# Performance work log

Measured on AMD Instinct MI355X. Metric: run time of the kernel, lower is better.

Reference implementation:

```python
import jax, jax.numpy as jnp
import numpy as np

N = 100000      # nodes
E = 1600000     # edges (before self-loops)
F_IN = 128      # dataset.num_features
H1 = 128        # hidden_channels/2
H2 = 256        # hidden_channels
C = 40          # dataset.num_classes
EPS = 1e-5      # BatchNorm eps
NEG_SLOPE = 0.2 # GATConv leaky_relu slope


def setup_inputs() -> dict:
    key = jax.random.key(0)
    ks = jax.random.split(key, 12)
    p = lambda k, shape: jax.random.normal(k, shape, jnp.float32) * 0.1
    x = jax.random.normal(ks[0], (N, F_IN), jnp.float32)
    edge_index = jax.random.randint(ks[1], (2, E), 0, N, dtype=jnp.int64)
    return dict(
        x=x, edge_index=edge_index,
        w1=p(ks[2], (F_IN, H1)), as1=p(ks[3], (H1,)), ad1=p(ks[4], (H1,)), b1=jnp.zeros(H1, jnp.float32),
        g1=jnp.ones(H1, jnp.float32), be1=jnp.zeros(H1, jnp.float32), rm1=jnp.zeros(H1, jnp.float32), rv1=jnp.ones(H1, jnp.float32),
        w2=p(ks[5], (H1, H2)), as2=p(ks[6], (H2,)), ad2=p(ks[7], (H2,)), b2=jnp.zeros(H2, jnp.float32),
        g2=jnp.ones(H2, jnp.float32), be2=jnp.zeros(H2, jnp.float32), rm2=jnp.zeros(H2, jnp.float32), rv2=jnp.ones(H2, jnp.float32),
        w3=p(ks[8], (H2, C)), as3=p(ks[9], (C,)), ad3=p(ks[10], (C,)), b3=jnp.zeros(C, jnp.float32),
    )


def gat_conv(x, src, dst, W, a_src, a_dst, b):
    """PyG GATConv (heads=1, add_self_loops already applied to src/dst)."""
    h = x @ W                                  # [N, F_out]
    alpha_src = h @ a_src                      # [N]
    alpha_dst = h @ a_dst                      # [N]
    logits = jax.nn.leaky_relu(alpha_src[src] + alpha_dst[dst], NEG_SLOPE)  # [E']
    # segment softmax over incoming edges of each dst node
    m = jax.ops.segment_max(logits, dst, num_segments=N)
    e = jnp.exp(logits - m[dst])
    denom = jax.ops.segment_sum(e, dst, num_segments=N)
    alpha = e / denom[dst]                     # [E']
    out = jax.ops.segment_sum(h[src] * alpha[:, None], dst, num_segments=N)
    return out + b


def bn_eval(x, gamma, beta, mean, var):
    return (x - mean) * jax.lax.rsqrt(var + EPS) * gamma + beta


def reference(x, edge_index,
              w1, as1, ad1, b1, g1, be1, rm1, rv1,
              w2, as2, ad2, b2, g2, be2, rm2, rv2,
              w3, as3, ad3, b3):
    # add self-loops once (PyG GATConv default add_self_loops=True)
    loop = jnp.arange(N, dtype=edge_index.dtype)
    src = jnp.concatenate([edge_index[0], loop])
    dst = jnp.concatenate([edge_index[1], loop])
    # eval mode: dropout is identity, BN uses running stats
    h = gat_conv(x, src, dst, w1, as1, ad1, b1)
    h = jnp.tanh(bn_eval(h, g1, be1, rm1, rv1))
    h = gat_conv(h, src, dst, w2, as2, ad2, b2)
    h = jnp.tanh(bn_eval(h, g2, be2, rm2, rv2))
    return gat_conv(h, src, dst, w3, as3, ad3, b3)
```

## Files before the change

### kernel.cpp

```cpp
#include <hip/hip_runtime.h>
#include <hip/hip_bf16.h>
#include <cstddef>

#define N_NODES 100000
#define E_EDGES 1600000
#define TOT_EDGES (E_EDGES + N_NODES)
#define NEG_SLOPE 0.2f
#define BN_EPS 1e-5f
#define NBKT ((N_NODES + 255) / 256)
#define NBA 512

typedef __attribute__((ext_vector_type(8))) short short8;
typedef __attribute__((ext_vector_type(4))) float f32x4;
typedef __attribute__((ext_vector_type(2))) float f32x2;
typedef __attribute__((ext_vector_type(4))) int int32x4;
typedef __attribute__((ext_vector_type(2))) int int32x2;

#if defined(__has_builtin)
#if __has_builtin(__builtin_amdgcn_make_buffer_rsrc) && __has_builtin(__builtin_amdgcn_raw_buffer_load_b128)
#define HAVE_BUFRSRC 1
#endif
#if __has_builtin(__builtin_amdgcn_make_buffer_rsrc) && __has_builtin(__builtin_amdgcn_raw_buffer_load_b64)
#define HAVE_BUF64 1
#endif
#endif

__device__ __forceinline__ unsigned short f2bf(float f) {
    union { float f; unsigned u; } c; c.f = f;
    unsigned u = c.u;
    u += 0x7fffu + ((u >> 16) & 1u);
    return (unsigned short)(u >> 16);
}
__device__ __forceinline__ float bf2f(unsigned short h) {
    union { unsigned u; float f; } c; c.u = ((unsigned)h) << 16;
    return c.f;
}
__device__ __forceinline__ unsigned short f2h(float f) {
    union { _Float16 h; unsigned short u; } c; c.h = (_Float16)f; return c.u;
}
__device__ __forceinline__ float lrelu(float t) {
    return (t > 0.f) ? t : NEG_SLOPE * t;
}
__device__ __forceinline__ float tanh_fast(float x) {
    float e = __expf(2.f * x);
    return 1.f - 2.f / (e + 1.f);
}
__device__ __forceinline__ unsigned short pk_fp8(float a, float b) {
    unsigned v;
    asm volatile("v_cvt_pk_fp8_f32 %0, %1, %2" : "=v"(v) : "v"(a), "v"(b));
    return (unsigned short)v;
}
__device__ __forceinline__ f32x2 unpk_fp8(unsigned u) {
    f32x2 r;
    asm volatile("v_cvt_pk_f32_fp8 %0, %1" : "=v"(r) : "v"(u));
    return r;
}

__device__ __forceinline__ float wave_sum63(float x) {
    x += __int_as_float(__builtin_amdgcn_update_dpp(0, __float_as_int(x), 0x111, 0xf, 0xf, true));
    x += __int_as_float(__builtin_amdgcn_update_dpp(0, __float_as_int(x), 0x112, 0xf, 0xf, true));
    x += __int_as_float(__builtin_amdgcn_update_dpp(0, __float_as_int(x), 0x114, 0xf, 0xf, true));
    x += __int_as_float(__builtin_amdgcn_update_dpp(0, __float_as_int(x), 0x118, 0xf, 0xf, true));
    x += __int_as_float(__builtin_amdgcn_update_dpp(0, __float_as_int(x), 0x142, 0xf, 0xf, true));
    x += __int_as_float(__builtin_amdgcn_update_dpp(0, __float_as_int(x), 0x143, 0xf, 0xf, true));
    return x;
}
__device__ __forceinline__ float wave_sum_bcast(float x) {
    return __int_as_float(__builtin_amdgcn_readlane(__float_as_int(wave_sum63(x)), 63));
}


__global__ __launch_bounds__(256) void csr_hist(const int* __restrict__ ei,
                                                int* __restrict__ bh) {
    __shared__ int h[NBKT];
    int t = threadIdx.x;
    for (int b = t; b < NBKT; b += 256) h[b] = 0;
    __syncthreads();
    int idx = blockIdx.x * 256 + t;
    const int stride = NBA * 256;
    for (int e = idx; e < TOT_EDGES; e += stride) {
        int d = (e < E_EDGES) ? ei[E_EDGES + e] : (e - E_EDGES);
        atomicAdd(&h[((unsigned)d) >> 8], 1);
    }
    __syncthreads();
    for (int b = t; b < NBKT; b += 256) bh[blockIdx.x * NBKT + b] = h[b];
}

__global__ __launch_bounds__(512) void csr_scan_blocks(int* __restrict__ bh,
                                                       int* __restrict__ totals) {
    __shared__ int s[NBA];
    int t = threadIdx.x, bin = blockIdx.x;
    int v = bh[t * NBKT + bin];
    s[t] = v;
    __syncthreads();
    for (int off = 1; off < NBA; off <<= 1) {
        int y = (t >= off) ? s[t - off] : 0;
        __syncthreads();
        s[t] += y;
        __syncthreads();
    }
    bh[t * NBKT + bin] = s[t] - v;
    if (t == NBA - 1) totals[bin] = s[t];
}

__global__ __launch_bounds__(512) void csr_scan_buckets(const int* __restrict__ totals,
                                                        int* __restrict__ starts) {
    __shared__ int s[512];
    int t = threadIdx.x;
    int v = (t < NBKT) ? totals[t] : 0;
    s[t] = v;
    __syncthreads();
    for (int off = 1; off < 512; off <<= 1) {
        int y = (t >= off) ? s[t - off] : 0;
        __syncthreads();
        s[t] += y;
        __syncthreads();
    }
    if (t < NBKT) starts[t] = s[t] - v;
    if (t == 0) starts[NBKT] = TOT_EDGES;
}

__global__ __launch_bounds__(256) void csr_scatter(const int* __restrict__ ei,
                                                   const int* __restrict__ bh,
                                                   const int* __restrict__ starts,
                                                   int* __restrict__ pairs) {
    __shared__ int wp[NBKT];
    int t = threadIdx.x;
    for (int b = t; b < NBKT; b += 256)
        wp[b] = starts[b] + bh[blockIdx.x * NBKT + b];
    __syncthreads();
    int idx = blockIdx.x * 256 + t;
    const int stride = NBA * 256;
    for (int e = idx; e < TOT_EDGES; e += stride) {
        int s, d;
        if (e < E_EDGES) { s = ei[e]; d = ei[E_EDGES + e]; }
        else             { s = e - E_EDGES; d = s; }
        int pos = atomicAdd(&wp[((unsigned)d) >> 8], 1);
        pairs[pos] = s | ((d & 255) << 20);
    }
}

__global__ __launch_bounds__(256) void csr_build(const int* __restrict__ pairs,
                                                 const int* __restrict__ starts,
                                                 int* __restrict__ row_ptr,
                                                 int* __restrict__ src_sorted) {
    __shared__ int nh[256];
    __shared__ int sc[256];
    __shared__ int wp[256];
    int k = blockIdx.x, t = threadIdx.x;
    int bs = starts[k], be = starts[k + 1];
    nh[t] = 0;
    __syncthreads();
    for (int i = bs + t; i < be; i += 256)
        atomicAdd(&nh[((unsigned)pairs[i]) >> 20], 1);
    __syncthreads();
    int v = nh[t];
    sc[t] = v;
    __syncthreads();
    for (int off = 1; off < 256; off <<= 1) {
        int y = (t >= off) ? sc[t - off] : 0;
        __syncthreads();
        sc[t] += y;
        __syncthreads();
    }
    int excl = sc[t] - v;
    int node = k * 256 + t;
    if (node <= N_NODES) row_ptr[node] = bs + excl;
    wp[t] = bs + excl;
    __syncthreads();
    for (int i = bs + t; i < be; i += 256) {
        unsigned p = (unsigned)pairs[i];
        int pos = atomicAdd(&wp[p >> 20], 1);
        src_sorted[pos] = (int)(p & 0xFFFFFu);
    }
}

__global__ __launch_bounds__(256) void wprep_all(
    const float* __restrict__ w1, const float* __restrict__ w2, const float* __restrict__ w3,
    const float* __restrict__ as1, const float* __restrict__ ad1,
    const float* __restrict__ as2, const float* __restrict__ ad2,
    const float* __restrict__ as3, const float* __restrict__ ad3,
    unsigned short* __restrict__ w1th, unsigned short* __restrict__ w1tl,
    unsigned short* __restrict__ w2th, unsigned short* __restrict__ w2tl,
    unsigned short* __restrict__ w3th, unsigned short* __restrict__ w3tl,
    unsigned short* __restrict__ ab1h, unsigned short* __restrict__ ab1l,
    unsigned short* __restrict__ ab3h, unsigned short* __restrict__ ab3l,
    float* __restrict__ ws2f, float* __restrict__ wd2f) {
    const int T1 = 128 * 128, T2 = 256 * 128, T3 = 48 * 256;
    const int W = T1 + T2 + T3;
    int idx = blockIdx.x * 256 + threadIdx.x;
    if (idx < W) {
        float v; unsigned short* th; unsigned short* tl; int o;
        if (idx < T1) {
            int n = idx / 128, k = idx % 128;
            v = w1[k * 128 + n]; th = w1th; tl = w1tl; o = idx;
        } else if (idx < T1 + T2) {
            int i = idx - T1; int n = i / 128, k = i % 128;
            v = w2[k * 256 + n]; th = w2th; tl = w2tl; o = i;
        } else {
            int i = idx - T1 - T2; int n = i / 256, k = i % 256;
            v = (n < 40) ? w3[k * 40 + n] : 0.f; th = w3th; tl = w3tl; o = i;
        }
        unsigned short h = f2bf(v);
        th[o] = h;
        tl[o] = f2bf(v - bf2f(h));
        return;
    }
    int j = idx - W;
    if (j < 2048) {
        int r = j / 128, k = j % 128;
        float v = 0.f;
        if (r < 2) {
            const float* a = r ? ad1 : as1;
            const float* wr = w1 + (size_t)k * 128;
            for (int n = 0; n < 128; n++) v += wr[n] * a[n];
        }
        unsigned short h = f2bf(v);
        ab1h[j] = h; ab1l[j] = f2bf(v - bf2f(h));
    } else if (j < 2048 + 4096) {
        int i = j - 2048; int r = i / 256, k = i % 256;
        float v = 0.f;
        if (r < 2) {
            const float* a = r ? ad3 : as3;
            const float* wr = w3 + (size_t)k * 40;
            for (int n = 0; n < 40; n++) v += wr[n] * a[n];
        }
        unsigned short h = f2bf(v);
        ab3h[i] = h; ab3l[i] = f2bf(v - bf2f(h));
    } else if (j < 2048 + 4096 + 256) {
        int i = j - 2048 - 4096; int r = i / 128, k = i % 128;
        const float* a = r ? ad2 : as2;
        const float* wr = w2 + (size_t)k * 256;
        float v = 0.f;
        for (int n = 0; n < 256; n++) v += wr[n] * a[n];
        if (r == 0) ws2f[k] = v; else wd2f[k] = v;
    }
}

template<int K, int NTILES, int MWAVES, int NWAVES, int NACT, bool ASPLIT, bool ALPHA, bool BNT, bool CFRAG, bool CHALF, bool AF32>
__global__ __launch_bounds__(256) void mfma_gemm(
    const unsigned short* __restrict__ Ahi, const unsigned short* __restrict__ Alo,
    const unsigned short* __restrict__ BThi, const unsigned short* __restrict__ BTlo,
    const unsigned short* __restrict__ ABh, const unsigned short* __restrict__ ABl,
    unsigned short* __restrict__ Chi, int ldc,
    const float* __restrict__ bias, const float* __restrict__ gamma,
    const float* __restrict__ beta, const float* __restrict__ rmean,
    const float* __restrict__ rvar,
    float* __restrict__ asrc, float* __restrict__ adst, int M)
{
    int lane = threadIdx.x & 63;
    int wave = threadIdx.x >> 6;
    int quad = lane >> 4;
    int l16  = lane & 15;
    long mbase = (long)blockIdx.x * (64 * MWAVES) + (long)(wave / NWAVES) * 64;
    int n0 = ((wave % NWAVES) + blockIdx.y * NWAVES) * (NTILES * 16);
    bool aw = ((wave % NWAVES) == 0) && (blockIdx.y == 0);
    const size_t CSTRIDE = (size_t)M * 32;

    size_t roff[4];
#pragma unroll
    for (int i = 0; i < 4; i++) {
        long r = mbase + i * 16 + l16;
        if (r > M - 1) r = M - 1;
        roff[i] = AF32 ? ((size_t)r * K + (size_t)(quad * 8))
                       : ((size_t)r * 32 + (size_t)(quad * 8));
    }
    const unsigned short* bh[NTILES]; const unsigned short* bl[NTILES];
#pragma unroll
    for (int j = 0; j < NTILES; j++) {
        long n = n0 + j * 16 + l16;
        bh[j] = BThi + n * K; bl[j] = BTlo + n * K;
    }
    const unsigned short* bah = nullptr; const unsigned short* bal = nullptr;
    if constexpr (ALPHA) { bah = ABh + (size_t)l16 * K; bal = ABl + (size_t)l16 * K; }
    const int ko = quad * 8;

    f32x4 acc[4][NTILES];
    f32x4 acca[4];
#pragma unroll
    for (int i = 0; i < 4; i++) {
        acca[i] = (f32x4){0.f, 0.f, 0.f, 0.f};
#pragma unroll
        for (int j = 0; j < NTILES; j++)
            acc[i][j] = (f32x4){0.f, 0.f, 0.f, 0.f};
    }

    for (int kc = 0; kc < K / 32; kc++) {
        const int k0 = kc * 32;
        short8 vah[4], vall[4], vbh[NTILES], vbl[NTILES];
#pragma unroll
        for (int i = 0; i < 4; i++) {
            if constexpr (AF32) {
                const float* xf = (const float*)Ahi;
                const float* pa = xf + roff[i] + kc * 32;
                f32x4 va = *(const f32x4*)pa;
                f32x4 vb = *(const f32x4*)(pa + 4);
#pragma unroll
                for (int q = 0; q < 8; q++) {
                    float v = (q < 4) ? va[q] : vb[q - 4];
                    unsigned short h = f2bf(v);
                    vah[i][q] = (short)h;
                    vall[i][q] = (short)f2bf(v - bf2f(h));
                }
            } else {
                const unsigned short* Ah = Ahi + (size_t)kc * CSTRIDE;
                vah[i] = *(const short8*)(Ah + roff[i]);
                if constexpr (ASPLIT) {
                    const unsigned short* Al = Alo + (size_t)kc * CSTRIDE;
                    vall[i] = *(const short8*)(Al + roff[i]);
                }
            }
        }
#pragma unroll
        for (int j = 0; j < NTILES; j++) {
            vbh[j] = *(const short8*)(bh[j] + k0 + ko);
            vbl[j] = *(const short8*)(bl[j] + k0 + ko);
        }
#pragma unroll
        for (int i = 0; i < 4; i++)
#pragma unroll
            for (int j = 0; j < NTILES; j++) {
                acc[i][j] = __builtin_amdgcn_mfma_f32_16x16x32_bf16(vah[i], vbh[j], acc[i][j], 0, 0, 0);
                acc[i][j] = __builtin_amdgcn_mfma_f32_16x16x32_bf16(vah[i], vbl[j], acc[i][j], 0, 0, 0);
                if constexpr (ASPLIT)
                    acc[i][j] = __builtin_amdgcn_mfma_f32_16x16x32_bf16(vall[i], vbh[j], acc[i][j], 0, 0, 0);
            }
        if constexpr (ALPHA) {
            if (aw) {
                short8 vbah = *(const short8*)(bah + k0 + ko);
                short8 vbal = *(const short8*)(bal + k0 + ko);
#pragma unroll
                for (int i = 0; i < 4; i++) {
                    acca[i] = __builtin_amdgcn_mfma_f32_16x16x32_bf16(vah[i], vbah, acca[i], 0, 0, 0);
                    acca[i] = __builtin_amdgcn_mfma_f32_16x16x32_bf16(vah[i], vbal, acca[i], 0, 0, 0);
                    if constexpr (ASPLIT)
                        acca[i] = __builtin_amdgcn_mfma_f32_16x16x32_bf16(vall[i], vbah, acca[i], 0, 0, 0);
                }
            }
        }
    }

#pragma unroll
    for (int i = 0; i < 4; i++)
#pragma unroll
        for (int j = 0; j < NTILES; j++) {
            int col = n0 + j * 16 + l16;
            float bb = 0.f, rs = 1.f, gg = 1.f, bt = 0.f, rm = 0.f;
            if constexpr (BNT) {
                bb = bias[col]; gg = gamma[col]; bt = beta[col];
                rm = rmean[col]; rs = rsqrtf(rvar[col] + BN_EPS);
            }
#pragma unroll
            for (int r = 0; r < 4; r++) {
                long row = mbase + i * 16 + quad * 4 + r;
                if (row < M && col < NACT) {
                    float v = acc[i][j][r];
                    if constexpr (BNT) v = tanh_fast((v + bb - rm) * rs * gg + bt);
                    if constexpr (CFRAG) {
                        Chi[(size_t)(col >> 5) * CSTRIDE + (size_t)row * 32 + (col & 31)] = f2bf(v);
                    } else {
                        Chi[row * ldc + col] = CHALF ? f2h(v) : f2bf(v);
                    }
                }
            }
        }
    if constexpr (ALPHA) {
        if (aw) {
#pragma unroll
            for (int i = 0; i < 4; i++)
#pragma unroll
                for (int r = 0; r < 4; r++) {
                    long row = mbase + i * 16 + quad * 4 + r;
                    if (row < M) {
                        float v = acca[i][r];
                        if (l16 == 0) asrc[row] = v;
                        else if (l16 == 1) adst[row] = v;
                    }
                }
        }
    }
}

__global__ __launch_bounds__(256) void gemm23_fused(
    const unsigned short* __restrict__ Ahi,
    const unsigned short* __restrict__ B2h, const unsigned short* __restrict__ B2l,
    const float* __restrict__ bias, const float* __restrict__ gamma,
    const float* __restrict__ beta, const float* __restrict__ rmean,
    const float* __restrict__ rvar,
    const unsigned short* __restrict__ B3h, const unsigned short* __restrict__ B3l,
    const unsigned short* __restrict__ AB3h, const unsigned short* __restrict__ AB3l,
    unsigned short* __restrict__ h3,
    float* __restrict__ asrc, float* __restrict__ adst, int M)
{
    constexpr int LW = 40;
    __shared__ unsigned short o2l[8 * 64 * LW];

    int lane = threadIdx.x & 63;
    int wave = threadIdx.x >> 6;
    int quad = lane >> 4;
    int l16  = lane & 15;
    long mbase = (long)blockIdx.x * 64;
    const size_t CSTRIDE = (size_t)M * 32;
    const int ko = quad * 8;

    size_t roff[4];
#pragma unroll
    for (int i = 0; i < 4; i++) {
        long r = mbase + i * 16 + l16;
        if (r > M - 1) r = M - 1;
        roff[i] = (size_t)r * 32 + (size_t)ko;
    }
    int n0 = wave * 64;
    const unsigned short* bh[4]; const unsigned short* bl[4];
#pragma unroll
    for (int j = 0; j < 4; j++) {
        long n = n0 + j * 16 + l16;
        bh[j] = B2h + n * 128; bl[j] = B2l + n * 128;
    }

    f32x4 acc[4][4];
#pragma unroll
    for (int i = 0; i < 4; i++)
#pragma unroll
        for (int j = 0; j < 4; j++)
            acc[i][j] = (f32x4){0.f, 0.f, 0.f, 0.f};

    for (int kc = 0; kc < 4; kc++) {
        const int k0 = kc * 32;
        const unsigned short* Ah = Ahi + (size_t)kc * CSTRIDE;
        short8 vah[4], vbh[4], vbl[4];
#pragma unroll
        for (int i = 0; i < 4; i++) vah[i] = *(const short8*)(Ah + roff[i]);
#pragma unroll
        for (int j = 0; j < 4; j++) {
            vbh[j] = *(const short8*)(bh[j] + k0 + ko);
            vbl[j] = *(const short8*)(bl[j] + k0 + ko);
        }
#pragma unroll
        for (int i = 0; i < 4; i++)
#pragma unroll
            for (int j = 0; j < 4; j++) {
                acc[i][j] = __builtin_amdgcn_mfma_f32_16x16x32_bf16(vah[i], vbh[j], acc[i][j], 0, 0, 0);
                acc[i][j] = __builtin_amdgcn_mfma_f32_16x16x32_bf16(vah[i], vbl[j], acc[i][j], 0, 0, 0);
            }
    }

#pragma unroll
    for (int j = 0; j < 4; j++) {
        int col = n0 + j * 16 + l16;
        float bb = bias[col], gg = gamma[col], bt = beta[col];
        float rm = rmean[col], rs = rsqrtf(rvar[col] + BN_EPS);
        int cbase = (col >> 5) * 64 * LW + (col & 31);
#pragma unroll
        for (int i = 0; i < 4; i++)
#pragma unroll
            for (int r = 0; r < 4; r++) {
                int li = i * 16 + quad * 4 + r;
                float v = tanh_fast((acc[i][j][r] + bb - rm) * rs * gg + bt);
                o2l[cbase + li * LW] = f2bf(v);
            }
    }
    __syncthreads();

    const unsigned short* b3h[3]; const unsigned short* b3l[3];
#pragma unroll
    for (int j = 0; j < 3; j++) {
        long n = j * 16 + l16;
        b3h[j] = B3h + n * 256; b3l[j] = B3l + n * 256;
    }
    const unsigned short* bah = AB3h + (size_t)l16 * 256;
    const unsigned short* bal = AB3l + (size_t)l16 * 256;
    int lrow = wave * 16 + l16;

    f32x4 acc3[3], acca;
#pragma unroll
    for (int j = 0; j < 3; j++) acc3[j] = (f32x4){0.f, 0.f, 0.f, 0.f};
    acca = (f32x4){0.f, 0.f, 0.f, 0.f};

    for (int kc = 0; kc < 8; kc++) {
        const int k0 = kc * 32;
        short8 a = *(const short8*)(o2l + (kc * 64 + lrow) * LW + ko);
        short8 vbh[3], vbl[3];
#pragma unroll
        for (int j = 0; j < 3; j++) {
            vbh[j] = *(const short8*)(b3h[j] + k0 + ko);
            vbl[j] = *(const short8*)(b3l[j] + k0 + ko);
        }
#pragma unroll
        for (int j = 0; j < 3; j++) {
            acc3[j] = __builtin_amdgcn_mfma_f32_16x16x32_bf16(a, vbh[j], acc3[j], 0, 0, 0);
            acc3[j] = __builtin_amdgcn_mfma_f32_16x16x32_bf16(a, vbl[j], acc3[j], 0, 0, 0);
        }
        short8 vbah = *(const short8*)(bah + k0 + ko);
        short8 vbal = *(const short8*)(bal + k0 + ko);
        acca = __builtin_amdgcn_mfma_f32_16x16x32_bf16(a, vbah, acca, 0, 0, 0);
        acca = __builtin_amdgcn_mfma_f32_16x16x32_bf16(a, vbal, acca, 0, 0, 0);
    }

#pragma unroll
    for (int j = 0; j < 3; j++) {
        int col = j * 16 + l16;
#pragma unroll
        for (int r = 0; r < 4; r++) {
            long row = mbase + wave * 16 + quad * 4 + r;
            if (row < M) h3[(size_t)row * 64 + col] = f2h(acc3[j][r]);
        }
    }
#pragma unroll
    for (int r = 0; r < 4; r++) {
        long row = mbase + wave * 16 + quad * 4 + r;
        if (row < M) {
            if (l16 == 0) asrc[row] = acca[r];
            else if (l16 == 1) adst[row] = acca[r];
        }
    }
}

template<int MODE>
__global__ __launch_bounds__(256) void gat_agg_wide(
    const unsigned short* __restrict__ hsrc,
    const float* __restrict__ asrc, const float* __restrict__ adst,
    const int* __restrict__ row_ptr, const int* __restrict__ src_sorted,
    const float* __restrict__ bias, const float* __restrict__ gamma,
    const float* __restrict__ beta, const float* __restrict__ rmean,
    const float* __restrict__ rvar,
    const float* __restrict__ wsn, const float* __restrict__ wdn,
    unsigned short* __restrict__ ohi,
    float* __restrict__ outf,
    float* __restrict__ asrc_n, float* __restrict__ adst_n)
{
    constexpr int SH  = (MODE == 0) ? 8 : 7;
    constexpr int BPL = (MODE == 0) ? 16 : 8;
    constexpr int NF  = (MODE == 2) ? 4 : 8;

    __shared__ __align__(16) float2 esw[4][64];
    __shared__ __align__(16) float red[4][4][132];

    int wave = threadIdx.x >> 6;
    int lane = threadIdx.x & 63;
    int node = blockIdx.x * 4 + wave;
    if (node >= N_NODES) return;

    int start = row_ptr[node];
    int end = row_ptr[node + 1];
    int deg = end - start;
    float ad = adst[node];
    int sub = lane >> 4;
    int foff = (lane & 15) * BPL;
    int tpos = (lane & 3) * 16 + (lane >> 2);

#if defined(HAVE_BUFRSRC) && defined(HAVE_BUF64)
    auto rsrc = __builtin_amdgcn_make_buffer_rsrc((void*)hsrc, (short)0,
                                                  N_NODES << SH, 0x00020000);
#endif

    float acc[NF];
#pragma unroll
    for (int i = 0; i < NF; i++) acc[i] = 0.f;

    auto ld = [&](int vo) {
        if constexpr (MODE == 0) {
#if defined(HAVE_BUFRSRC) && defined(HAVE_BUF64)
            return __builtin_amdgcn_raw_buffer_load_b128(rsrc, vo, 0, 0);
#else
            return *reinterpret_cast<const int32x4*>(
                reinterpret_cast<const char*>(hsrc) + (unsigned)vo);
#endif
        } else {
#if defined(HAVE_BUFRSRC) && defined(HAVE_BUF64)
            return __builtin_amdgcn_raw_buffer_load_b64(rsrc, vo, 0, 0);
#else
            return *reinterpret_cast<const int32x2*>(
                reinterpret_cast<const char*>(hsrc) + (unsigned)vo);
#endif
        }
    };
    auto fmaN = [&](auto u, float ww) {
        if constexpr (MODE == 0) {
            union { decltype(u) v; unsigned w[4]; } c; c.v = u;
#pragma unroll
            for (int i = 0; i < 4; i++) {
                union { unsigned u; _Float16 h[2]; } t; t.u = c.w[i];
                acc[2 * i]     += ww * (float)t.h[0];
                acc[2 * i + 1] += ww * (float)t.h[1];
            }
        } else if constexpr (MODE == 1) {
            union { decltype(u) v; unsigned w[2]; } c; c.v = u;
#pragma unroll
            for (int i = 0; i < 2; i++) {
                f32x2 lo = unpk_fp8(c.w[i]);
                f32x2 hi = unpk_fp8(c.w[i] >> 16);
                acc[4 * i]     += ww * lo.x;
                acc[4 * i + 1] += ww * lo.y;
                acc[4 * i + 2] += ww * hi.x;
                acc[4 * i + 3] += ww * hi.y;
            }
        } else {
            union { decltype(u) v; unsigned w[2]; } c; c.v = u;
#pragma unroll
            for (int i = 0; i < 2; i++) {
                union { unsigned u; _Float16 h[2]; } t; t.u = c.w[i];
                acc[2 * i]     += ww * (float)t.h[0];
                acc[2 * i + 1] += ww * (float)t.h[1];
            }
        }
    };
    auto gather = [&](int nst) {
        const float2* ep = &esw[wave][sub * 16];
#pragma unroll
        for (int b = 0; b < 4; b++) {
            int s0 = b * 4;
            if (s0 < nst) {
                f32x4 p01 = *(const f32x4*)(ep + s0);
                f32x4 p23 = *(const f32x4*)(ep + s0 + 2);
                bool g1 = s0 + 1 < nst, g2 = s0 + 2 < nst, g3 = s0 + 3 < nst;
                auto u0 = ld(__float_as_int(p01.x) + foff);
                decltype(u0) u1, u2, u3;
                if (g1) u1 = ld(__float_as_int(p01.z) + foff);
                if (g2) u2 = ld(__float_as_int(p23.x) + foff);
                if (g3) u3 = ld(__float_as_int(p23.z) + foff);
                fmaN(u0, p01.y);
                if (g1) fmaN(u1, p01.w);
                if (g2) fmaN(u2, p23.y);
                if (g3) fmaN(u3, p23.w);
            }
        }
    };

    if (deg <= 64) {
        int e = start + lane;
        int s = 0; float w = 0.f;
        if (e < end) { s = src_sorted[e]; w = __expf(lrelu(asrc[s] + ad)); }
        float dsum = wave_sum_bcast(w);
        esw[wave][tpos] = make_float2(__int_as_float(s << SH), w * (1.0f / dsum));
        gather((deg + 3) >> 2);
    } else {
        float part = 0.f;
        for (int cs = start; cs < end; cs += 64) {
            int e = cs + lane;
            if (e < end) part += __expf(lrelu(asrc[src_sorted[e]] + ad));
        }
        float inv = 1.0f / wave_sum_bcast(part);
        for (int cs = start; cs < end; cs += 64) {
            int e = cs + lane;
            int s = 0; float w = 0.f;
            if (e < end) { s = src_sorted[e]; w = __expf(lrelu(asrc[s] + ad)) * inv; }
            esw[wave][tpos] = make_float2(__int_as_float(s << SH), w);
            gather((min(64, end - cs) + 3) >> 2);
        }
    }

    if constexpr (MODE == 2) {
        *reinterpret_cast<f32x4*>(&red[wave][sub][(lane & 15) * 4]) =
            (f32x4){acc[0], acc[1], acc[2], acc[3]};
        float t = 0.f;
#pragma unroll
        for (int g = 0; g < 4; g++) t += red[wave][g][lane];
        if (lane < 40) outf[(size_t)node * 40 + lane] = t + bias[lane];
    } else {
        f32x4* dst = reinterpret_cast<f32x4*>(&red[wave][sub][(lane & 15) * 8]);
        dst[0] = (f32x4){acc[0], acc[1], acc[2], acc[3]};
        dst[1] = (f32x4){acc[4], acc[5], acc[6], acc[7]};
        f32x2 tsum = (f32x2){0.f, 0.f};
#pragma unroll
        for (int g = 0; g < 4; g++)
            tsum += *reinterpret_cast<const f32x2*>(&red[wave][g][lane * 2]);

        if constexpr (MODE == 0) {
            float vals[2];
#pragma unroll
            for (int v = 0; v < 2; v++) {
                int f = lane * 2 + v;
                float val = tsum[v] + bias[f];
                float rs = rsqrtf(rvar[f] + BN_EPS);
                vals[v] = tanh_fast((val - rmean[f]) * rs * gamma[f] + beta[f]);
            }
            ohi[(size_t)node * 64 + lane] = pk_fp8(vals[0], vals[1]);
            float ps = vals[0] * wsn[lane * 2] + vals[1] * wsn[lane * 2 + 1];
            float pd = vals[0] * wdn[lane * 2] + vals[1] * wdn[lane * 2 + 1];
            ps = wave_sum63(ps);
            pd = wave_sum63(pd);
            if (lane == 63) { asrc_n[node] = ps; adst_n[node] = pd; }
        } else {
            const size_t CSTRIDE = (size_t)N_NODES * 32;
            unsigned w0 = (unsigned)f2bf(tsum[0]) | ((unsigned)f2bf(tsum[1]) << 16);
            size_t a = (size_t)(lane >> 4) * CSTRIDE + (size_t)node * 32 + ((lane * 2) & 31);
            *reinterpret_cast<unsigned*>(ohi + a) = w0;
        }
    }
}


static inline size_t align256(size_t x) { return (x + 255) & ~(size_t)255; }

extern "C" void kernel_launch(void* const* d_in, const int* in_sizes, int n_in,
                              void* d_out, int out_size, void* d_ws, size_t ws_size,
                              hipStream_t stream) {
    const float* x   = (const float*)d_in[0];
    const int* ei    = (const int*)d_in[1];
    const float* w1  = (const float*)d_in[2];
    const float* as1 = (const float*)d_in[3];
    const float* ad1 = (const float*)d_in[4];
    const float* b1  = (const float*)d_in[5];
    const float* g1  = (const float*)d_in[6];
    const float* be1 = (const float*)d_in[7];
    const float* rm1 = (const float*)d_in[8];
    const float* rv1 = (const float*)d_in[9];
    const float* w2  = (const float*)d_in[10];
    const float* as2 = (const float*)d_in[11];
    const float* ad2 = (const float*)d_in[12];
    const float* b2  = (const float*)d_in[13];
    const float* g2  = (const float*)d_in[14];
    const float* be2 = (const float*)d_in[15];
    const float* rm2 = (const float*)d_in[16];
    const float* rv2 = (const float*)d_in[17];
    const float* w3  = (const float*)d_in[18];
    const float* as3 = (const float*)d_in[19];
    const float* ad3 = (const float*)d_in[20];
    const float* b3  = (const float*)d_in[21];
    float* out = (float*)d_out;

    const size_t P128 = align256((size_t)N_NODES * 128 * 2);
    const size_t P256 = align256((size_t)N_NODES * 256 * 2);

    char* p = (char*)d_ws;
    char* regA = p; p += P256;
    char* regB = p; p += P256;
    unsigned short* o1p  = (unsigned short*)regA;
    unsigned short* h3h  = (unsigned short*)regA;
    unsigned short* h1h  = (unsigned short*)regB;
    unsigned short* g2hi = (unsigned short*)regB;
    int* pairs  = (int*)regB;
    int* bhist  = (int*)(regB + align256((size_t)TOT_EDGES * 4));
    int* totals = (int*)((char*)bhist + align256((size_t)NBA * NBKT * 4));
    int* starts = (int*)((char*)totals + align256((size_t)NBKT * 4));

    float* asrcA = (float*)p; p += align256((size_t)N_NODES * 4);
    float* adstA = (float*)p; p += align256((size_t)N_NODES * 4);
    float* asrcB = (float*)p; p += align256((size_t)N_NODES * 4);
    float* adstB = (float*)p; p += align256((size_t)N_NODES * 4);
    int* row_ptr   = (int*)p; p += align256((size_t)(N_NODES + 1) * 4);
    int* src_sorted = (int*)p; p += align256((size_t)TOT_EDGES * 4);
    unsigned short* w1th = (unsigned short*)p; p += align256(128 * 128 * 2);
    unsigned short* w1tl = (unsigned short*)p; p += align256(128 * 128 * 2);
    unsigned short* w2th = (unsigned short*)p; p += align256(256 * 128 * 2);
    unsigned short* w2tl = (unsigned short*)p; p += align256(256 * 128 * 2);
    unsigned short* w3th = (unsigned short*)p; p += align256(48 * 256 * 2);
    unsigned short* w3tl = (unsigned short*)p; p += align256(48 * 256 * 2);
    unsigned short* ab1h = (unsigned short*)p; p += align256(16 * 128 * 2);
    unsigned short* ab1l = (unsigned short*)p; p += align256(16 * 128 * 2);
    unsigned short* ab3h = (unsigned short*)p; p += align256(16 * 256 * 2);
    unsigned short* ab3l = (unsigned short*)p; p += align256(16 * 256 * 2);
    float* ws2f = (float*)p; p += align256(128 * 4);
    float* wd2f = (float*)p; p += align256(128 * 4);

    const int WTOT = 128 * 128 + 256 * 128 + 48 * 256 + 2048 + 4096 + 256;

    wprep_all<<<(WTOT + 255) / 256, 256, 0, stream>>>(
        w1, w2, w3, as1, ad1, as2, ad2, as3, ad3,
        w1th, w1tl, w2th, w2tl, w3th, w3tl,
        ab1h, ab1l, ab3h, ab3l, ws2f, wd2f);

    csr_hist<<<NBA, 256, 0, stream>>>(ei, bhist);
    csr_scan_blocks<<<NBKT, 512, 0, stream>>>(bhist, totals);
    csr_scan_buckets<<<1, 512, 0, stream>>>(totals, starts);
    csr_scatter<<<NBA, 256, 0, stream>>>(ei, bhist, starts, pairs);
    csr_build<<<NBKT, 256, 0, stream>>>(pairs, starts, row_ptr, src_sorted);

    const int NWB = (N_NODES + 3) / 4;
    const int G64 = (N_NODES + 63) / 64;

    mfma_gemm<128, 2, 1, 4, 128, true, true, false, false, true, true><<<G64, 256, 0, stream>>>(
        (const unsigned short*)x, nullptr, w1th, w1tl, ab1h, ab1l, h1h, 128,
        nullptr, nullptr, nullptr, nullptr, nullptr, asrcA, adstA, N_NODES);
    gat_agg_wide<0><<<NWB, 256, 0, stream>>>(
        h1h, asrcA, adstA, row_ptr, src_sorted,
        b1, g1, be1, rm1, rv1, ws2f, wd2f,
        o1p, nullptr, asrcB, adstB);

    gat_agg_wide<1><<<NWB, 256, 0, stream>>>(
        o1p, asrcB, adstB, row_ptr, src_sorted,
        nullptr, nullptr, nullptr, nullptr, nullptr, nullptr, nullptr,
        g2hi, nullptr, nullptr, nullptr);

    gemm23_fused<<<G64, 256, 0, stream>>>(
        g2hi, w2th, w2tl, b2, g2, be2, rm2, rv2,
        w3th, w3tl, ab3h, ab3l, h3h, asrcA, adstA, N_NODES);

    gat_agg_wide<2><<<NWB, 256, 0, stream>>>(
        h3h, asrcA, adstA, row_ptr, src_sorted,
        b3, nullptr, nullptr, nullptr, nullptr, nullptr, nullptr,
        nullptr, out, nullptr, nullptr);
}
```

Baseline: 463.4 us.

## Use 8 waves per block in fused GEMM2/3 and split second GEMM by task

The fused layer-2/layer-3 GEMM kernel now launches 512 threads per 64-row tile. Each wave computes 32 output columns of GEMM2 instead of 64, which halves per-wave accumulator registers. The second stage is repartitioned so each wave handles one of four tasks (three 16-column output tiles or the attention projections) across 32 rows, instead of each wave doing all of them for 16 rows. The intent is more latency hiding and lower register pressure. The cost is that the A tiles are loaded redundantly by more waves and the weight streams are split differently.

```diff
diff --git a/kernel.cpp b/kernel.cpp
--- a/kernel.cpp
+++ b/kernel.cpp
@@ -381,7 +381,7 @@
     }
 }
 
-__global__ __launch_bounds__(256) void gemm23_fused(
+__global__ __launch_bounds__(512) void gemm23_fused(
     const unsigned short* __restrict__ Ahi,
     const unsigned short* __restrict__ B2h, const unsigned short* __restrict__ B2l,
     const float* __restrict__ bias, const float* __restrict__ gamma,
@@ -410,43 +410,44 @@
         if (r > M - 1) r = M - 1;
         roff[i] = (size_t)r * 32 + (size_t)ko;
     }
-    int n0 = wave * 64;
-    const unsigned short* bh[4]; const unsigned short* bl[4];
-#pragma unroll
-    for (int j = 0; j < 4; j++) {
+    int n0 = wave * 32;
+    const unsigned short* bh[2]; const unsigned short* bl[2];
+#pragma unroll
+    for (int j = 0; j < 2; j++) {
         long n = n0 + j * 16 + l16;
         bh[j] = B2h + n * 128; bl[j] = B2l + n * 128;
     }
 
-    f32x4 acc[4][4];
+    f32x4 acc[4][2];
 #pragma unroll
     for (int i = 0; i < 4; i++)
 #pragma unroll
-        for (int j = 0; j < 4; j++)
+        for (int j = 0; j < 2; j++)
             acc[i][j] = (f32x4){0.f, 0.f, 0.f, 0.f};
 
+#pragma unroll
     for (int kc = 0; kc < 4; kc++) {
         const int k0 = kc * 32;
         const unsigned short* Ah = Ahi + (size_t)kc * CSTRIDE;
-        short8 vah[4], vbh[4], vbl[4];
+        short8 vah[4], vbh[2], vbl[2];
 #pragma unroll
         for (int i = 0; i < 4; i++) vah[i] = *(const short8*)(Ah + roff[i]);
 #pragma unroll
-        for (int j = 0; j < 4; j++) {
+        for (int j = 0; j < 2; j++) {
             vbh[j] = *(const short8*)(bh[j] + k0 + ko);
             vbl[j] = *(const short8*)(bl[j] + k0 + ko);
         }
 #pragma unroll
         for (int i = 0; i < 4; i++)
 #pragma unroll
-            for (int j = 0; j < 4; j++) {
+            for (int j = 0; j < 2; j++) {
                 acc[i][j] = __builtin_amdgcn_mfma_f32_16x16x32_bf16(vah[i], vbh[j], acc[i][j], 0, 0, 0);
                 acc[i][j] = __builtin_amdgcn_mfma_f32_16x16x32_bf16(vah[i], vbl[j], acc[i][j], 0, 0, 0);
             }
     }
 
 #pragma unroll
-    for (int j = 0; j < 4; j++) {
+    for (int j = 0; j < 2; j++) {
         int col = n0 + j * 16 + l16;
         float bb = bias[col], gg = gamma[col], bt = beta[col];
         float rm = rmean[col], rs = rsqrtf(rvar[col] + BN_EPS);
@@ -462,57 +463,58 @@
     }
     __syncthreads();
 
-    const unsigned short* b3h[3]; const unsigned short* b3l[3];
-#pragma unroll
-    for (int j = 0; j < 3; j++) {
-        long n = j * 16 + l16;
-        b3h[j] = B3h + n * 256; b3l[j] = B3l + n * 256;
-    }
-    const unsigned short* bah = AB3h + (size_t)l16 * 256;
-    const unsigned short* bal = AB3l + (size_t)l16 * 256;
-    int lrow = wave * 16 + l16;
-
-    f32x4 acc3[3], acca;
-#pragma unroll
-    for (int j = 0; j < 3; j++) acc3[j] = (f32x4){0.f, 0.f, 0.f, 0.f};
-    acca = (f32x4){0.f, 0.f, 0.f, 0.f};
-
+    int rh   = wave >> 2;
+    int task = wave & 3;
+    int lrow0 = rh * 32 + l16;
+    int lrow1 = rh * 32 + 16 + l16;
+
+    const unsigned short* p3h;
+    const unsigned short* p3l;
+    if (task < 3) {
+        p3h = B3h + (size_t)(task * 16 + l16) * 256;
+        p3l = B3l + (size_t)(task * 16 + l16) * 256;
+    } else {
+        p3h = AB3h + (size_t)l16 * 256;
+        p3l = AB3l + (size_t)l16 * 256;
+    }
+
+    f32x4 a3[2];
+    a3[0] = (f32x4){0.f, 0.f, 0.f, 0.f};
+    a3[1] = (f32x4){0.f, 0.f, 0.f, 0.f};
+
+#pragma unroll 2
     for (int kc = 0; kc < 8; kc++) {
         const int k0 = kc * 32;
-        short8 a = *(const short8*)(o2l + (kc * 64 + lrow) * LW + ko);
-        short8 vbh[3], vbl[3];
-#pragma unroll
-        for (int j = 0; j < 3; j++) {
-            vbh[j] = *(const short8*)(b3h[j] + k0 + ko);
-            vbl[j] = *(const short8*)(b3l[j] + k0 + ko);
-        }
-#pragma unroll
-        for (int j = 0; j < 3; j++) {
-            acc3[j] = __builtin_amdgcn_mfma_f32_16x16x32_bf16(a, vbh[j], acc3[j], 0, 0, 0);
-            acc3[j] = __builtin_amdgcn_mfma_f32_16x16x32_bf16(a, vbl[j], acc3[j], 0, 0, 0);
-        }
-        short8 vbah = *(const short8*)(bah + k0 + ko);
-        short8 vbal = *(const short8*)(bal + k0 + ko);
-        acca = __builtin_amdgcn_mfma_f32_16x16x32_bf16(a, vbah, acca, 0, 0, 0);
-        acca = __builtin_amdgcn_mfma_f32_16x16x32_bf16(a, vbal, acca, 0, 0, 0);
-    }
-
-#pragma unroll
-    for (int j = 0; j < 3; j++) {
-        int col = j * 16 + l16;
-#pragma unroll
-        for (int r = 0; r < 4; r++) {
-            long row = mbase + wave * 16 + quad * 4 + r;
-            if (row < M) h3[(size_t)row * 64 + col] = f2h(acc3[j][r]);
-        }
-    }
-#pragma unroll
-    for (int r = 0; r < 4; r++) {
-        long row = mbase + wave * 16 + quad * 4 + r;
-        if (row < M) {
-            if (l16 == 0) asrc[row] = acca[r];
-            else if (l16 == 1) adst[row] = acca[r];
-        }
+        short8 a0 = *(const short8*)(o2l + (kc * 64 + lrow0) * LW + ko);
+        short8 a1 = *(const short8*)(o2l + (kc * 64 + lrow1) * LW + ko);
+        short8 vh = *(const short8*)(p3h + k0 + ko);
+        short8 vl = *(const short8*)(p3l + k0 + ko);
+        a3[0] = __builtin_amdgcn_mfma_f32_16x16x32_bf16(a0, vh, a3[0], 0, 0, 0);
+        a3[0] = __builtin_amdgcn_mfma_f32_16x16x32_bf16(a0, vl, a3[0], 0, 0, 0);
+        a3[1] = __builtin_amdgcn_mfma_f32_16x16x32_bf16(a1, vh, a3[1], 0, 0, 0);
+        a3[1] = __builtin_amdgcn_mfma_f32_16x16x32_bf16(a1, vl, a3[1], 0, 0, 0);
+    }
+
+    if (task < 3) {
+        int col = task * 16 + l16;
+#pragma unroll
+        for (int i = 0; i < 2; i++)
+#pragma unroll
+            for (int r = 0; r < 4; r++) {
+                long row = mbase + rh * 32 + i * 16 + quad * 4 + r;
+                if (row < M) h3[(size_t)row * 64 + col] = f2h(a3[i][r]);
+            }
+    } else {
+#pragma unroll
+        for (int i = 0; i < 2; i++)
+#pragma unroll
+            for (int r = 0; r < 4; r++) {
+                long row = mbase + rh * 32 + i * 16 + quad * 4 + r;
+                if (row < M) {
+                    if (l16 == 0) asrc[row] = a3[i][r];
+                    else if (l16 == 1) adst[row] = a3[i][r];
+                }
+            }
     }
 }
 
@@ -783,7 +785,7 @@
         nullptr, nullptr, nullptr, nullptr, nullptr, nullptr, nullptr,
         g2hi, nullptr, nullptr, nullptr);
 
-    gemm23_fused<<<G64, 256, 0, stream>>>(
+    gemm23_fused<<<G64, 512, 0, stream>>>(
         g2hi, w2th, w2tl, b2, g2, be2, rm2, rv2,
         w3th, w3tl, ab3h, ab3l, h3h, asrcA, adstA, N_NODES);
 
```

After: 440.6 us. 1.05x faster.
